# Optimization experiments

Hardware: AMD Instinct MI355X
Metric: run time of the kernel (lower is better)

## Reference

```python
import jax, jax.numpy as jnp
import numpy as np

BN_EPS = 1e-5


def _conv1x1(x, w, b=None):
    # x: [B,C,H,W], w: [O,C] (1x1 conv kernel squeezed)
    y = jnp.einsum('bchw,oc->bohw', x, w)
    if b is not None:
        y = y + b[None, :, None, None]
    return y


def _maxpool2(x):
    B, C, H, W = x.shape
    return x.reshape(B, C, H // 2, 2, W // 2, 2).max(axis=(3, 5))


def setup_inputs() -> dict:
    key = jax.random.key(0)
    ks = jax.random.split(key, 14)
    B, C, H, W = 8, 128, 64, 64
    IC = C // 2  # inter_channels
    s = 0.05
    f32 = jnp.float32
    return {
        'x': jax.random.normal(ks[0], (B, C, H, W), f32),
        'w1': jax.random.normal(ks[1], (IC, C), f32) * s,
        'b1': jax.random.normal(ks[2], (IC,), f32) * s,
        'w3': jax.random.normal(ks[3], (IC, C), f32) * s,
        'b3': jax.random.normal(ks[4], (IC,), f32) * s,
        'w4': jax.random.normal(ks[5], (IC, C), f32) * s,
        'b4': jax.random.normal(ks[6], (IC,), f32) * s,
        'w5': jax.random.normal(ks[7], (2 * IC,), f32) * s,  # conv5_pr, no bias
        'w2': jax.random.normal(ks[8], (C, IC), f32) * s,  # zero-init in torch; randomized for a non-trivial baseline
        'b2': jax.random.normal(ks[9], (C,), f32) * s,
        'bn_gamma': 1.0 + jax.random.normal(ks[10], (C,), f32) * 0.1,
        'bn_beta': jax.random.normal(ks[11], (C,), f32) * 0.1,
        'bn_mean': jax.random.normal(ks[12], (C,), f32) * 0.1,
        'bn_var': jax.random.uniform(ks[13], (C,), f32, 0.5, 1.5),
    }


def reference(x, w1, b1, w3, b3, w4, b4, w5, w2, b2, bn_gamma, bn_beta, bn_mean, bn_var):
    B, C, H, W = x.shape
    IC = C // 2
    N = H * W            # query positions
    # value branch: conv1 -> maxpool -> [B, M, IC]
    xg = _maxpool2(_conv1x1(x, w1, b1)).reshape(B, IC, -1)  # [B, IC, M]
    M = xg.shape[-1]
    xg = xg.transpose(0, 2, 1)  # [B, M, IC]
    # affinity: relu(w5 . cat(xt_i, xp_j)) is separable -> avoid [B,2IC,N,M] blowup
    xt = _conv1x1(x, w3, b3).reshape(B, IC, N)              # [B, IC, N]
    xp = _maxpool2(_conv1x1(x, w4, b4)).reshape(B, IC, M)   # [B, IC, M]
    wt, wp = w5[:IC], w5[IC:]
    logits = jnp.einsum('c,bcn->bn', wt, xt)[:, :, None] + \
             jnp.einsum('c,bcm->bm', wp, xp)[:, None, :]    # [B, N, M]
    feats = jax.nn.relu(logits) / M
    # aggregate
    y = jnp.einsum('bnm,bmi->bni', feats, xg)               # [B, N, IC]
    y = y.transpose(0, 2, 1).reshape(B, IC, H, W)
    # conv2 + batchnorm (eval mode, running stats)
    y = _conv1x1(y, w2, b2)
    inv = jax.lax.rsqrt(bn_var + BN_EPS)
    y = (y - bn_mean[None, :, None, None]) * (bn_gamma * inv)[None, :, None, None] + bn_beta[None, :, None, None]
    return y + x
```

## Files before the change

### kernel.cpp

```cpp
#include <hip/hip_runtime.h>

typedef unsigned int u32;
typedef unsigned short u16;

#define Cn 128
#define ICn 64
#define Nn 4096
#define Mn 1024

typedef __attribute__((ext_vector_type(8))) short s8v;
typedef __attribute__((ext_vector_type(4))) float f4v;

__device__ __forceinline__ float bf2f(u16 u){ union{u32 i; float f;} v; v.i = ((u32)u) << 16; return v.f; }
__device__ __forceinline__ u16 f2bf(float f){ union{float f; u32 i;} v; v.f = f; u32 r = v.i + 0x7fffu + ((v.i >> 16) & 1u); return (u16)(r >> 16); }
__device__ __forceinline__ u32 pk2(float lo, float hi){ return (u32)f2bf(lo) | ((u32)f2bf(hi) << 16); }

__global__ __launch_bounds__(256) void k_conv(
    const float* __restrict__ x,
    const float* __restrict__ w1, const float* __restrict__ b1,
    const float* __restrict__ w3, const float* __restrict__ b3,
    const float* __restrict__ w4, const float* __restrict__ b4,
    const float* __restrict__ w5, const float* __restrict__ w2,
    float* __restrict__ t_o, float* __restrict__ p_o, float* __restrict__ g_o)
{
    const int tile = blockIdx.x;
    const int r  = tile >> 1;
    const int wb = tile & 1;
    const int b  = blockIdx.y;
    const int tid = threadIdx.x;

    __shared__ __align__(16) u16 smem[32768];
    u16* xsT = smem;
    u16* w1t = smem + 8704;
    u16* w4t = smem + 17408;
    float* ph = (float*)&smem[26112];
    u16* w2t = smem + 8704;
    u16* xgr = smem + 17920;
    float* u3s = (float*)&smem[30464];

    #pragma unroll
    for (int it = 0; it < 8; ++it) {
        int f = tid + 256 * it;
        int c = f >> 4, rem = f & 15;
        int rl = rem >> 3, wq = rem & 7;
        const float* src = x + ((size_t)(b * Cn + c)) * Nn + (2 * r + rl) * 64 + 32 * wb + 4 * wq;
        float4 v = *(const float4*)src;
        int lp0 = rl * 32 + 4 * wq;
        int cS = c ^ (wq << 3);
        xsT[(lp0 + 0) * 136 + cS] = f2bf(v.x);
        xsT[(lp0 + 1) * 136 + cS] = f2bf(v.y);
        xsT[(lp0 + 2) * 136 + cS] = f2bf(v.z);
        xsT[(lp0 + 3) * 136 + cS] = f2bf(v.w);
    }
    #pragma unroll
    for (int it = 0; it < 4; ++it) {
        int f = tid + 256 * it;
        int ic = f >> 4, cq = f & 15;
        const float4* s1 = (const float4*)&w1[f * 8];
        const float4* s4 = (const float4*)&w4[f * 8];
        float4 a0 = s1[0], a1v = s1[1];
        float4 d0 = s4[0], d1v = s4[1];
        uint4 A, D;
        A.x = pk2(a0.x, a0.y); A.y = pk2(a0.z, a0.w); A.z = pk2(a1v.x, a1v.y); A.w = pk2(a1v.z, a1v.w);
        D.x = pk2(d0.x, d0.y); D.y = pk2(d0.z, d0.w); D.z = pk2(d1v.x, d1v.y); D.w = pk2(d1v.z, d1v.w);
        *(uint4*)&w1t[ic * 136 + 8 * cq] = A;
        *(uint4*)&w4t[ic * 136 + 8 * cq] = D;
    }
    if (tid < 128) {
        float s = 0.f;
        #pragma unroll 16
        for (int ic = 0; ic < 64; ++ic) s += w5[ic] * w3[ic * Cn + tid];
        u3s[tid] = s;
    } else if (tid == 128) {
        float s = 0.f;
        #pragma unroll 16
        for (int ic = 0; ic < 64; ++ic) s += w5[ic] * b3[ic];
        u3s[128] = s;
    }
    __syncthreads();

    const int lane = tid & 63;
    const int wv   = tid >> 6;
    const int col  = lane & 15;
    const int quad = lane >> 4;

    f4v acc1[4] = {}, acc4[4] = {};
    const u16* xrow = &xsT[(16 * wv + col) * 136];
    const int xsw = (((16 * wv + col) >> 2) & 7) << 3;
    #pragma unroll
    for (int kb = 0; kb < 4; ++kb) {
        s8v bx = *(const s8v*)&xrow[(kb * 32 + quad * 8) ^ xsw];
        #pragma unroll
        for (int icb = 0; icb < 4; ++icb) {
            s8v a1 = *(const s8v*)&w1t[(icb * 16 + col) * 136 + kb * 32 + quad * 8];
            s8v a4 = *(const s8v*)&w4t[(icb * 16 + col) * 136 + kb * 32 + quad * 8];
            acc1[icb] = __builtin_amdgcn_mfma_f32_16x16x32_bf16(a1, bx, acc1[icb], 0, 0, 0);
            acc4[icb] = __builtin_amdgcn_mfma_f32_16x16x32_bf16(a4, bx, acc4[icb], 0, 0, 0);
        }
    }
    __syncthreads();

    const int lp = 16 * wv + col;
    const int rl = lp >> 5, wl = lp & 31, pw = wl >> 1;
    const bool wr = (wl & 1) == 0;
    #pragma unroll
    for (int icb = 0; icb < 4; ++icb)
        #pragma unroll
        for (int reg = 0; reg < 4; ++reg) {
            float v = acc1[icb][reg];
            float vm = fmaxf(v, __shfl_xor(v, 1, 64));
            if (wr) ph[(rl * 16 + pw) * 68 + icb * 16 + quad * 4 + reg] = vm;
        }
    __syncthreads();

    #pragma unroll
    for (int it = 0; it < 4; ++it) {
        int e = tid + 256 * it;
        int pwq = e >> 6, ic = e & 63;
        float v = fmaxf(ph[pwq * 68 + ic], ph[(16 + pwq) * 68 + ic]) + b1[ic];
        xgr[pwq * 72 + ic] = f2bf(v);
    }
    {
        int px = tid >> 2, part = tid & 3;
        const int tsw = ((px >> 2) & 7) << 3;
        const u16* xr = &xsT[px * 136];
        float s = 0.f;
        #pragma unroll
        for (int cq = 0; cq < 4; ++cq) {
            int u = part * 32 + cq * 8;
            s8v xv = *(const s8v*)&xr[u ^ tsw];
            #pragma unroll
            for (int j = 0; j < 8; ++j) s += u3s[u + j] * bf2f((u16)xv[j]);
        }
        s += __shfl_xor(s, 1, 64);
        s += __shfl_xor(s, 2, 64);
        if (part == 0)
            t_o[(size_t)b * Nn + (2 * r + (px >> 5)) * 64 + 32 * wb + (px & 31)] = s + u3s[128];
    }
    __syncthreads();

    #pragma unroll
    for (int it = 0; it < 4; ++it) {
        int f = tid + 256 * it;
        int co = f >> 3, iq = f & 7;
        const float4* s2 = (const float4*)&w2[f * 8];
        float4 a0 = s2[0], a1v = s2[1];
        uint4 V;
        V.x = pk2(a0.x, a0.y); V.y = pk2(a0.z, a0.w); V.z = pk2(a1v.x, a1v.y); V.w = pk2(a1v.z, a1v.w);
        *(uint4*)&w2t[co * 72 + 8 * iq] = V;
    }
    #pragma unroll
    for (int icb = 0; icb < 4; ++icb)
        #pragma unroll
        for (int reg = 0; reg < 4; ++reg) {
            float v = acc4[icb][reg];
            float vm = fmaxf(v, __shfl_xor(v, 1, 64));
            if (wr) ph[(rl * 16 + pw) * 68 + icb * 16 + quad * 4 + reg] = vm;
        }
    __syncthreads();

    #pragma unroll
    for (int cob2 = 0; cob2 < 2; ++cob2) {
        int cob = 2 * wv + cob2;
        f4v gacc = {};
        #pragma unroll
        for (int kb = 0; kb < 2; ++kb) {
            s8v a  = *(const s8v*)&xgr[col * 72 + kb * 32 + quad * 8];
            s8v bb = *(const s8v*)&w2t[(cob * 16 + col) * 72 + kb * 32 + quad * 8];
            gacc = __builtin_amdgcn_mfma_f32_16x16x32_bf16(a, bb, gacc, 0, 0, 0);
        }
        #pragma unroll
        for (int reg = 0; reg < 4; ++reg) {
            int pwr = quad * 4 + reg;
            int m = r * 32 + wb * 16 + pwr;
            g_o[((size_t)b * Mn + m) * 128 + cob * 16 + col] = gacc[reg];
        }
    }

    if (tid < 16) {
        float s = 0.f;
        #pragma unroll 8
        for (int ic = 0; ic < 64; ++ic) {
            float pv = fmaxf(ph[tid * 68 + ic], ph[(16 + tid) * 68 + ic]) + b4[ic];
            s += w5[64 + ic] * pv;
        }
        p_o[(size_t)b * Mn + r * 32 + wb * 16 + tid] = s;
    }
}

__global__ __launch_bounds__(256) void k_rank(
    const float* __restrict__ p, float* __restrict__ ps, int* __restrict__ perm)
{
    const int seg = blockIdx.x;
    const int b   = blockIdx.y;
    const int tid = threadIdx.x;
    __shared__ float pls[1024];
    #pragma unroll
    for (int it = 0; it < 4; ++it) pls[tid + 256 * it] = p[b * 1024 + tid + 256 * it];
    __syncthreads();
    const int m = seg * 32 + (tid >> 3);
    const int sub = tid & 7;
    const float key = pls[m];
    int rank = 0;
    #pragma unroll 8
    for (int jj = 0; jj < 128; ++jj) {
        int j = sub + jj * 8;
        float v = pls[j];
        rank += (v < key || (v == key && j < m)) ? 1 : 0;
    }
    rank += __shfl_xor(rank, 1, 64);
    rank += __shfl_xor(rank, 2, 64);
    rank += __shfl_xor(rank, 4, 64);
    if (sub == 0) {
        ps[b * 1024 + rank]   = key;
        perm[b * 1024 + rank] = m;
    }
}

__global__ __launch_bounds__(256) void k_scanA(
    const float* __restrict__ g, const float* __restrict__ ps, const int* __restrict__ perm,
    float* __restrict__ csa, float* __restrict__ csb)
{
    const int seg = blockIdx.x;
    const int b = blockIdx.y;
    const int tid = threadIdx.x;
    const int co = tid & 127, jh = tid >> 7;
    __shared__ float redA[2][128], redB[2][128];
    __shared__ float pl[32];
    __shared__ int   pml[32];
    if (tid < 32) { pl[tid] = ps[b * 1024 + seg * 32 + tid]; pml[tid] = perm[b * 1024 + seg * 32 + tid]; }
    __syncthreads();
    float sA = 0.f, sB = 0.f;
    for (int jj = jh * 16; jj < jh * 16 + 16; ++jj) {
        float gv = g[((size_t)b * Mn + pml[jj]) * 128 + co];
        sA += gv; sB += pl[jj] * gv;
    }
    redA[jh][co] = sA; redB[jh][co] = sB;
    __syncthreads();
    if (tid < 128) {
        csa[(b * 32 + seg) * 128 + tid] = redA[0][tid] + redA[1][tid];
        csb[(b * 32 + seg) * 128 + tid] = redB[0][tid] + redB[1][tid];
    }
}

__global__ __launch_bounds__(256) void k_scanC(
    const float* __restrict__ g, const float* __restrict__ ps, const int* __restrict__ perm,
    const float* __restrict__ csa, const float* __restrict__ csb,
    float* __restrict__ SA, float* __restrict__ SB)
{
    const int seg = blockIdx.x;
    const int b = blockIdx.y;
    const int tid = threadIdx.x;
    __shared__ float gs[32 * 128];
    __shared__ float pl[32];
    __shared__ int   pml[32];
    if (tid < 32) { pl[tid] = ps[b * 1024 + seg * 32 + tid]; pml[tid] = perm[b * 1024 + seg * 32 + tid]; }
    __syncthreads();
    for (int it = 0; it < 16; ++it) {
        int f = tid + 256 * it;
        int jj = f >> 7, co = f & 127;
        gs[jj * 128 + co] = g[((size_t)b * Mn + pml[jj]) * 128 + co];
    }
    __syncthreads();

    const int co = tid & 127;
    if (tid < 128) {
        float rA = 0.f;
        for (int s = seg + 1; s < 32; ++s) rA += csa[(b * 32 + s) * 128 + co];
        if (seg == 31) SA[((size_t)b * 1025 + 1024) * 128 + co] = 0.f;
        for (int jj = 31; jj >= 0; --jj) {
            rA += gs[jj * 128 + co];
            SA[((size_t)b * 1025 + seg * 32 + jj) * 128 + co] = rA;
        }
    } else {
        float rB = 0.f;
        for (int s = seg + 1; s < 32; ++s) rB += csb[(b * 32 + s) * 128 + co];
        if (seg == 31) SB[((size_t)b * 1025 + 1024) * 128 + co] = 0.f;
        for (int jj = 31; jj >= 0; --jj) {
            rB += pl[jj] * gs[jj * 128 + co];
            SB[((size_t)b * 1025 + seg * 32 + jj) * 128 + co] = rB;
        }
    }
}

__global__ __launch_bounds__(256) void k_final(
    const float* __restrict__ x, const float* __restrict__ t,
    const float* __restrict__ ps, const float* __restrict__ SA, const float* __restrict__ SB,
    const float* __restrict__ b2, const float* __restrict__ gamma, const float* __restrict__ beta,
    const float* __restrict__ mean, const float* __restrict__ var,
    float* __restrict__ out)
{
    const int nt = blockIdx.x;
    const int b = blockIdx.y;
    const int tid = threadIdx.x;
    const int n0 = nt * 128;
    __shared__ float psl[1024];
    __shared__ float tl[128];
    __shared__ int   kl[128];
    __shared__ float sc[128], bs[128];
    __shared__ float sa_s[32][129], sb_s[32][129];

    for (int it = 0; it < 4; ++it) psl[tid + 256 * it] = ps[b * 1024 + tid + 256 * it];
    __syncthreads();
    if (tid < 128) {
        float tv = t[(size_t)b * Nn + n0 + tid];
        tl[tid] = tv;
        float key = -tv;
        int lo = 0, hi = 1024;
        while (lo < hi) { int mid = (lo + hi) >> 1; if (psl[mid] > key) hi = mid; else lo = mid + 1; }
        kl[tid] = lo;
    } else {
        int co = tid - 128;
        float s = gamma[co] * rsqrtf(var[co] + 1e-5f);
        sc[co] = s;
        bs[co] = (b2[co] - mean[co]) * s + beta[co];
    }
    __syncthreads();

    const float invM = 1.0f / 1024.0f;
    for (int sub = 0; sub < 4; ++sub) {
        for (int it = 0; it < 16; ++it) {
            int f = tid + 256 * it;
            int rowl = f >> 7, co = f & 127;
            int k = kl[sub * 32 + rowl];
            sa_s[rowl][co] = SA[((size_t)b * 1025 + k) * 128 + co];
            sb_s[rowl][co] = SB[((size_t)b * 1025 + k) * 128 + co];
        }
        __syncthreads();
        for (int it = 0; it < 4; ++it) {
            int f = tid + 256 * it;
            int co = f >> 3, nn0 = (f & 7) * 4;
            size_t gidx = ((size_t)b * Cn + co) * Nn + n0 + sub * 32 + nn0;
            float4 xv = *(const float4*)&x[gidx];
            float scv = sc[co], bsv = bs[co];
            float4 o;
            float v0 = (tl[sub*32+nn0+0] * sa_s[nn0+0][co] + sb_s[nn0+0][co]) * invM;
            float v1 = (tl[sub*32+nn0+1] * sa_s[nn0+1][co] + sb_s[nn0+1][co]) * invM;
            float v2 = (tl[sub*32+nn0+2] * sa_s[nn0+2][co] + sb_s[nn0+2][co]) * invM;
            float v3 = (tl[sub*32+nn0+3] * sa_s[nn0+3][co] + sb_s[nn0+3][co]) * invM;
            o.x = v0 * scv + bsv + xv.x;
            o.y = v1 * scv + bsv + xv.y;
            o.z = v2 * scv + bsv + xv.z;
            o.w = v3 * scv + bsv + xv.w;
            *(float4*)&out[gidx] = o;
        }
        __syncthreads();
    }
}

extern "C" void kernel_launch(void* const* d_in, const int* in_sizes, int n_in,
                              void* d_out, int out_size, void* d_ws, size_t ws_size,
                              hipStream_t stream)
{
    const float* x  = (const float*)d_in[0];
    const float* w1 = (const float*)d_in[1];
    const float* b1 = (const float*)d_in[2];
    const float* w3 = (const float*)d_in[3];
    const float* b3 = (const float*)d_in[4];
    const float* w4 = (const float*)d_in[5];
    const float* b4 = (const float*)d_in[6];
    const float* w5 = (const float*)d_in[7];
    const float* w2 = (const float*)d_in[8];
    const float* b2 = (const float*)d_in[9];
    const float* gm = (const float*)d_in[10];
    const float* bt = (const float*)d_in[11];
    const float* mn = (const float*)d_in[12];
    const float* vr = (const float*)d_in[13];
    float* out = (float*)d_out;

    float* ws = (float*)d_ws;
    const size_t FTOT = 3823872;
    if (ws_size < FTOT * sizeof(float)) return;

    float* t_w  = ws;
    float* p_w  = ws + 32768;
    float* ps_w = ws + 40960;
    int*   pm_w = (int*)(ws + 49152);
    float* g_w  = ws + 581632;
    float* csa  = ws + 1630208;
    float* csb  = ws + 1662976;
    float* SAp  = ws + 1695744;
    float* SBp  = ws + 2745344;

    k_conv <<<dim3(64, 8), 256, 0, stream>>>(x, w1, b1, w3, b3, w4, b4, w5, w2,
                                             t_w, p_w, g_w);
    k_rank <<<dim3(32, 8), 256, 0, stream>>>(p_w, ps_w, pm_w);
    k_scanA<<<dim3(32, 8), 256, 0, stream>>>(g_w, ps_w, pm_w, csa, csb);
    k_scanC<<<dim3(32, 8), 256, 0, stream>>>(g_w, ps_w, pm_w, csa, csb, SAp, SBp);
    k_final<<<dim3(32, 8), 256, 0, stream>>>(x, t_w, ps_w, SAp, SBp, b2, gm, bt, mn, vr, out);
}
```

Measured before the change: 129.4 us.

## Interleave SA/SB buffers, widen post-conv kernels to 512 threads, prefetch in final

SA/SB and csa/csb are interleaved into float2 arrays so scanC does both running sums in one thread, and final gathers both with one load. The rank, scanA, scanC and final kernels move to 512-thread blocks. The final kernel register-prefetches the next row group's SAB values and folds 1/M into the BN scale. k_conv loads two channels per thread and writes packed bf16 pairs, and the w5·w3 reduction is split into two accumulators. Together these aim to cut memory transactions and latency stalls, at the cost of more registers and half the threads idling in scanC.

Result: faster. 122.5 us (-5.4%).

```diff
diff --git a/kernel.cpp b/kernel.cpp
--- a/kernel.cpp
+++ b/kernel.cpp
@@ -39,18 +39,19 @@
     float* u3s = (float*)&smem[30464];
 
     #pragma unroll
-    for (int it = 0; it < 8; ++it) {
+    for (int it = 0; it < 4; ++it) {
         int f = tid + 256 * it;
-        int c = f >> 4, rem = f & 15;
+        int cp = f >> 4, rem = f & 15;
         int rl = rem >> 3, wq = rem & 7;
-        const float* src = x + ((size_t)(b * Cn + c)) * Nn + (2 * r + rl) * 64 + 32 * wb + 4 * wq;
-        float4 v = *(const float4*)src;
+        const float* src = x + ((size_t)(b * Cn + 2 * cp)) * Nn + (2 * r + rl) * 64 + 32 * wb + 4 * wq;
+        float4 v0 = *(const float4*)src;
+        float4 v1 = *(const float4*)(src + Nn);
         int lp0 = rl * 32 + 4 * wq;
-        int cS = c ^ (wq << 3);
-        xsT[(lp0 + 0) * 136 + cS] = f2bf(v.x);
-        xsT[(lp0 + 1) * 136 + cS] = f2bf(v.y);
-        xsT[(lp0 + 2) * 136 + cS] = f2bf(v.z);
-        xsT[(lp0 + 3) * 136 + cS] = f2bf(v.w);
+        int cS = (2 * cp) ^ (wq << 3);
+        *(u32*)&xsT[(lp0 + 0) * 136 + cS] = pk2(v0.x, v1.x);
+        *(u32*)&xsT[(lp0 + 1) * 136 + cS] = pk2(v0.y, v1.y);
+        *(u32*)&xsT[(lp0 + 2) * 136 + cS] = pk2(v0.z, v1.z);
+        *(u32*)&xsT[(lp0 + 3) * 136 + cS] = pk2(v0.w, v1.w);
     }
     #pragma unroll
     for (int it = 0; it < 4; ++it) {
@@ -67,10 +68,13 @@
         *(uint4*)&w4t[ic * 136 + 8 * cq] = D;
     }
     if (tid < 128) {
-        float s = 0.f;
-        #pragma unroll 16
-        for (int ic = 0; ic < 64; ++ic) s += w5[ic] * w3[ic * Cn + tid];
-        u3s[tid] = s;
+        float s0 = 0.f, s1 = 0.f;
+        #pragma unroll 8
+        for (int ic = 0; ic < 64; ic += 2) {
+            s0 += w5[ic]     * w3[ic * Cn + tid];
+            s1 += w5[ic + 1] * w3[(ic + 1) * Cn + tid];
+        }
+        u3s[tid] = s0 + s1;
     } else if (tid == 128) {
         float s = 0.f;
         #pragma unroll 16
@@ -188,7 +192,7 @@
     }
 }
 
-__global__ __launch_bounds__(256) void k_rank(
+__global__ __launch_bounds__(512) void k_rank(
     const float* __restrict__ p, float* __restrict__ ps, int* __restrict__ perm)
 {
     const int seg = blockIdx.x;
@@ -196,57 +200,60 @@
     const int tid = threadIdx.x;
     __shared__ float pls[1024];
     #pragma unroll
-    for (int it = 0; it < 4; ++it) pls[tid + 256 * it] = p[b * 1024 + tid + 256 * it];
-    __syncthreads();
-    const int m = seg * 32 + (tid >> 3);
-    const int sub = tid & 7;
+    for (int it = 0; it < 2; ++it) pls[tid + 512 * it] = p[b * 1024 + tid + 512 * it];
+    __syncthreads();
+    const int m = seg * 32 + (tid >> 4);
+    const int sub = tid & 15;
     const float key = pls[m];
     int rank = 0;
     #pragma unroll 8
-    for (int jj = 0; jj < 128; ++jj) {
-        int j = sub + jj * 8;
+    for (int jj = 0; jj < 64; ++jj) {
+        int j = sub + jj * 16;
         float v = pls[j];
         rank += (v < key || (v == key && j < m)) ? 1 : 0;
     }
     rank += __shfl_xor(rank, 1, 64);
     rank += __shfl_xor(rank, 2, 64);
     rank += __shfl_xor(rank, 4, 64);
+    rank += __shfl_xor(rank, 8, 64);
     if (sub == 0) {
         ps[b * 1024 + rank]   = key;
         perm[b * 1024 + rank] = m;
     }
 }
 
-__global__ __launch_bounds__(256) void k_scanA(
+__global__ __launch_bounds__(512) void k_scanA(
     const float* __restrict__ g, const float* __restrict__ ps, const int* __restrict__ perm,
-    float* __restrict__ csa, float* __restrict__ csb)
+    float2* __restrict__ csab)
 {
     const int seg = blockIdx.x;
     const int b = blockIdx.y;
     const int tid = threadIdx.x;
     const int co = tid & 127, jh = tid >> 7;
-    __shared__ float redA[2][128], redB[2][128];
+    __shared__ float redA[4][128], redB[4][128];
     __shared__ float pl[32];
     __shared__ int   pml[32];
     if (tid < 32) { pl[tid] = ps[b * 1024 + seg * 32 + tid]; pml[tid] = perm[b * 1024 + seg * 32 + tid]; }
     __syncthreads();
     float sA = 0.f, sB = 0.f;
-    for (int jj = jh * 16; jj < jh * 16 + 16; ++jj) {
+    #pragma unroll
+    for (int jj = jh * 8; jj < jh * 8 + 8; ++jj) {
         float gv = g[((size_t)b * Mn + pml[jj]) * 128 + co];
         sA += gv; sB += pl[jj] * gv;
     }
     redA[jh][co] = sA; redB[jh][co] = sB;
     __syncthreads();
     if (tid < 128) {
-        csa[(b * 32 + seg) * 128 + tid] = redA[0][tid] + redA[1][tid];
-        csb[(b * 32 + seg) * 128 + tid] = redB[0][tid] + redB[1][tid];
-    }
-}
-
-__global__ __launch_bounds__(256) void k_scanC(
+        float2 v;
+        v.x = (redA[0][tid] + redA[1][tid]) + (redA[2][tid] + redA[3][tid]);
+        v.y = (redB[0][tid] + redB[1][tid]) + (redB[2][tid] + redB[3][tid]);
+        csab[(b * 32 + seg) * 128 + tid] = v;
+    }
+}
+
+__global__ __launch_bounds__(512) void k_scanC(
     const float* __restrict__ g, const float* __restrict__ ps, const int* __restrict__ perm,
-    const float* __restrict__ csa, const float* __restrict__ csb,
-    float* __restrict__ SA, float* __restrict__ SB)
+    const float2* __restrict__ csab, float2* __restrict__ SAB)
 {
     const int seg = blockIdx.x;
     const int b = blockIdx.y;
@@ -256,36 +263,36 @@
     __shared__ int   pml[32];
     if (tid < 32) { pl[tid] = ps[b * 1024 + seg * 32 + tid]; pml[tid] = perm[b * 1024 + seg * 32 + tid]; }
     __syncthreads();
-    for (int it = 0; it < 16; ++it) {
-        int f = tid + 256 * it;
+    #pragma unroll
+    for (int it = 0; it < 8; ++it) {
+        int f = tid + 512 * it;
         int jj = f >> 7, co = f & 127;
         gs[jj * 128 + co] = g[((size_t)b * Mn + pml[jj]) * 128 + co];
     }
     __syncthreads();
 
-    const int co = tid & 127;
     if (tid < 128) {
-        float rA = 0.f;
-        for (int s = seg + 1; s < 32; ++s) rA += csa[(b * 32 + s) * 128 + co];
-        if (seg == 31) SA[((size_t)b * 1025 + 1024) * 128 + co] = 0.f;
+        const int co = tid;
+        float rA = 0.f, rB = 0.f;
+        #pragma unroll 4
+        for (int s2 = seg + 1; s2 < 32; ++s2) {
+            float2 v = csab[(b * 32 + s2) * 128 + co];
+            rA += v.x; rB += v.y;
+        }
+        if (seg == 31) SAB[((size_t)b * 1025 + 1024) * 128 + co] = make_float2(0.f, 0.f);
+        #pragma unroll
         for (int jj = 31; jj >= 0; --jj) {
-            rA += gs[jj * 128 + co];
-            SA[((size_t)b * 1025 + seg * 32 + jj) * 128 + co] = rA;
-        }
-    } else {
-        float rB = 0.f;
-        for (int s = seg + 1; s < 32; ++s) rB += csb[(b * 32 + s) * 128 + co];
-        if (seg == 31) SB[((size_t)b * 1025 + 1024) * 128 + co] = 0.f;
-        for (int jj = 31; jj >= 0; --jj) {
-            rB += pl[jj] * gs[jj * 128 + co];
-            SB[((size_t)b * 1025 + seg * 32 + jj) * 128 + co] = rB;
-        }
-    }
-}
-
-__global__ __launch_bounds__(256) void k_final(
+            float gv = gs[jj * 128 + co];
+            rA += gv;
+            rB += pl[jj] * gv;
+            SAB[((size_t)b * 1025 + seg * 32 + jj) * 128 + co] = make_float2(rA, rB);
+        }
+    }
+}
+
+__global__ __launch_bounds__(512) void k_final(
     const float* __restrict__ x, const float* __restrict__ t,
-    const float* __restrict__ ps, const float* __restrict__ SA, const float* __restrict__ SB,
+    const float* __restrict__ ps, const float2* __restrict__ SAB,
     const float* __restrict__ b2, const float* __restrict__ gamma, const float* __restrict__ beta,
     const float* __restrict__ mean, const float* __restrict__ var,
     float* __restrict__ out)
@@ -300,7 +307,8 @@
     __shared__ float sc[128], bs[128];
     __shared__ float sa_s[32][129], sb_s[32][129];
 
-    for (int it = 0; it < 4; ++it) psl[tid + 256 * it] = ps[b * 1024 + tid + 256 * it];
+    #pragma unroll
+    for (int it = 0; it < 2; ++it) psl[tid + 512 * it] = ps[b * 1024 + tid + 512 * it];
     __syncthreads();
     if (tid < 128) {
         float tv = t[(size_t)b * Nn + n0 + tid];
@@ -309,35 +317,52 @@
         int lo = 0, hi = 1024;
         while (lo < hi) { int mid = (lo + hi) >> 1; if (psl[mid] > key) hi = mid; else lo = mid + 1; }
         kl[tid] = lo;
-    } else {
+    } else if (tid < 256) {
         int co = tid - 128;
         float s = gamma[co] * rsqrtf(var[co] + 1e-5f);
-        sc[co] = s;
+        sc[co] = s * (1.0f / 1024.0f);
         bs[co] = (b2[co] - mean[co]) * s + beta[co];
     }
     __syncthreads();
 
-    const float invM = 1.0f / 1024.0f;
+    float2 pf[8], pf2[8];
+    {
+        #pragma unroll
+        for (int i2 = 0; i2 < 8; ++i2) {
+            int f = tid + 512 * i2;
+            int rowl = f >> 7, co = f & 127;
+            pf[i2] = SAB[((size_t)b * 1025 + kl[rowl]) * 128 + co];
+        }
+    }
     for (int sub = 0; sub < 4; ++sub) {
-        for (int it = 0; it < 16; ++it) {
-            int f = tid + 256 * it;
+        #pragma unroll
+        for (int i2 = 0; i2 < 8; ++i2) {
+            int f = tid + 512 * i2;
             int rowl = f >> 7, co = f & 127;
-            int k = kl[sub * 32 + rowl];
-            sa_s[rowl][co] = SA[((size_t)b * 1025 + k) * 128 + co];
-            sb_s[rowl][co] = SB[((size_t)b * 1025 + k) * 128 + co];
+            sa_s[rowl][co] = pf[i2].x;
+            sb_s[rowl][co] = pf[i2].y;
+        }
+        if (sub < 3) {
+            #pragma unroll
+            for (int i2 = 0; i2 < 8; ++i2) {
+                int f = tid + 512 * i2;
+                int rowl = f >> 7, co = f & 127;
+                pf2[i2] = SAB[((size_t)b * 1025 + kl[(sub + 1) * 32 + rowl]) * 128 + co];
+            }
         }
         __syncthreads();
-        for (int it = 0; it < 4; ++it) {
-            int f = tid + 256 * it;
+        #pragma unroll
+        for (int it = 0; it < 2; ++it) {
+            int f = tid + 512 * it;
             int co = f >> 3, nn0 = (f & 7) * 4;
             size_t gidx = ((size_t)b * Cn + co) * Nn + n0 + sub * 32 + nn0;
             float4 xv = *(const float4*)&x[gidx];
             float scv = sc[co], bsv = bs[co];
             float4 o;
-            float v0 = (tl[sub*32+nn0+0] * sa_s[nn0+0][co] + sb_s[nn0+0][co]) * invM;
-            float v1 = (tl[sub*32+nn0+1] * sa_s[nn0+1][co] + sb_s[nn0+1][co]) * invM;
-            float v2 = (tl[sub*32+nn0+2] * sa_s[nn0+2][co] + sb_s[nn0+2][co]) * invM;
-            float v3 = (tl[sub*32+nn0+3] * sa_s[nn0+3][co] + sb_s[nn0+3][co]) * invM;
+            float v0 = tl[sub*32+nn0+0] * sa_s[nn0+0][co] + sb_s[nn0+0][co];
+            float v1 = tl[sub*32+nn0+1] * sa_s[nn0+1][co] + sb_s[nn0+1][co];
+            float v2 = tl[sub*32+nn0+2] * sa_s[nn0+2][co] + sb_s[nn0+2][co];
+            float v3 = tl[sub*32+nn0+3] * sa_s[nn0+3][co] + sb_s[nn0+3][co];
             o.x = v0 * scv + bsv + xv.x;
             o.y = v1 * scv + bsv + xv.y;
             o.z = v2 * scv + bsv + xv.z;
@@ -345,6 +370,8 @@
             *(float4*)&out[gidx] = o;
         }
         __syncthreads();
+        #pragma unroll
+        for (int i2 = 0; i2 < 8; ++i2) pf[i2] = pf2[i2];
     }
 }
 
@@ -372,20 +399,18 @@
     const size_t FTOT = 3823872;
     if (ws_size < FTOT * sizeof(float)) return;
 
-    float* t_w  = ws;
-    float* p_w  = ws + 32768;
-    float* ps_w = ws + 40960;
-    int*   pm_w = (int*)(ws + 49152);
-    float* g_w  = ws + 581632;
-    float* csa  = ws + 1630208;
-    float* csb  = ws + 1662976;
-    float* SAp  = ws + 1695744;
-    float* SBp  = ws + 2745344;
+    float*  t_w  = ws;
+    float*  p_w  = ws + 32768;
+    float*  ps_w = ws + 40960;
+    int*    pm_w = (int*)(ws + 49152);
+    float*  g_w  = ws + 581632;
+    float2* csab = (float2*)(ws + 1630208);
+    float2* SAB  = (float2*)(ws + 1695744);
 
     k_conv <<<dim3(64, 8), 256, 0, stream>>>(x, w1, b1, w3, b3, w4, b4, w5, w2,
                                              t_w, p_w, g_w);
-    k_rank <<<dim3(32, 8), 256, 0, stream>>>(p_w, ps_w, pm_w);
-    k_scanA<<<dim3(32, 8), 256, 0, stream>>>(g_w, ps_w, pm_w, csa, csb);
-    k_scanC<<<dim3(32, 8), 256, 0, stream>>>(g_w, ps_w, pm_w, csa, csb, SAp, SBp);
-    k_final<<<dim3(32, 8), 256, 0, stream>>>(x, t_w, ps_w, SAp, SBp, b2, gm, bt, mn, vr, out);
-}
+    k_rank <<<dim3(32, 8), 512, 0, stream>>>(p_w, ps_w, pm_w);
+    k_scanA<<<dim3(32, 8), 512, 0, stream>>>(g_w, ps_w, pm_w, csab);
+    k_scanC<<<dim3(32, 8), 512, 0, stream>>>(g_w, ps_w, pm_w, csab, SAB);
+    k_final<<<dim3(32, 8), 512, 0, stream>>>(x, t_w, ps_w, SAB, b2, gm, bt, mn, vr, out);
+}
```
